# Optimization experiments

Measured on AMD Instinct MI355X. Metric: run time of the kernel, lower is better.

The kernel has to match this reference:

```python
import jax, jax.numpy as jnp
import numpy as np

N, DIM, HID, NCLS, E = 100000, 256, 16, 64, 3200000
NEG_SLOPE = 0.2


def setup_inputs() -> dict:
    key = jax.random.key(0)
    ks = jax.random.split(key, 10)
    x = jax.random.normal(ks[0], (N, DIM), dtype=jnp.float32)
    edge_index = jax.random.randint(ks[1], (2, E), 0, N, dtype=jnp.int64)
    # GATConv params (heads=1): glorot-ish scaled normals
    W1 = jax.random.normal(ks[2], (DIM, HID), dtype=jnp.float32) / np.sqrt(DIM)
    a_src1 = jax.random.normal(ks[3], (HID,), dtype=jnp.float32) / np.sqrt(HID)
    a_dst1 = jax.random.normal(ks[4], (HID,), dtype=jnp.float32) / np.sqrt(HID)
    b1 = jnp.zeros((HID,), dtype=jnp.float32)
    W2 = jax.random.normal(ks[5], (HID, NCLS), dtype=jnp.float32) / np.sqrt(HID)
    a_src2 = jax.random.normal(ks[6], (NCLS,), dtype=jnp.float32) / np.sqrt(NCLS)
    a_dst2 = jax.random.normal(ks[7], (NCLS,), dtype=jnp.float32) / np.sqrt(NCLS)
    b2 = jnp.zeros((NCLS,), dtype=jnp.float32)
    return {"x": x, "edge_index": edge_index, "W1": W1, "a_src1": a_src1,
            "a_dst1": a_dst1, "b1": b1, "W2": W2, "a_src2": a_src2,
            "a_dst2": a_dst2, "b2": b2}


def gat_conv(x, src, dst, W, a_s, a_d, b, n):
    # PyG GATConv, heads=1: h = x W; e_ij = LeakyReLU(a_s.h_j + a_d.h_i)
    h = x @ W                                   # [N, out]
    alpha_s = h @ a_s                           # [N]
    alpha_d = h @ a_d                           # [N]
    e = jax.nn.leaky_relu(alpha_s[src] + alpha_d[dst], NEG_SLOPE)  # [E]
    # softmax over edges grouped by destination node
    m = jax.ops.segment_max(e, dst, num_segments=n)
    m = jnp.where(jnp.isfinite(m), m, 0.0)
    ee = jnp.exp(e - m[dst])
    denom = jax.ops.segment_sum(ee, dst, num_segments=n)
    alpha = ee / denom[dst]                     # self-loops guarantee denom > 0
    out = jax.ops.segment_sum(h[src] * alpha[:, None], dst, num_segments=n)
    return out + b


def reference(x, edge_index, W1, a_src1, a_dst1, b1, W2, a_src2, a_dst2, b2):
    n = x.shape[0]
    loop = jnp.arange(n, dtype=edge_index.dtype)
    src = jnp.concatenate([edge_index[0], loop])  # add self-loops (PyG default)
    dst = jnp.concatenate([edge_index[1], loop])
    h = jax.nn.relu(gat_conv(x, src, dst, W1, a_src1, a_dst1, b1, n))
    # F.dropout treated as identity (inference / deterministic reference)
    out = gat_conv(h, src, dst, W2, a_src2, a_dst2, b2, n)
    return jax.nn.log_softmax(out, axis=1)
```

## Files before the change

### kernel.cpp

```cpp
#include <hip/hip_runtime.h>
#include <hip/hip_fp16.h>


#define DIM 256
#define HID 16
#define NCLS 64
#define NEG 0.2f
#define P1_CHUNK 4096
#define KITER 16
#define CAP 8704

typedef _Float16 f16x8 __attribute__((ext_vector_type(8)));
typedef float f32x4 __attribute__((ext_vector_type(4)));

#define PIN4(v) asm volatile("" : "+v"(v.x), "+v"(v.y), "+v"(v.z), "+v"(v.w))

__device__ __forceinline__ float lrelu(float v) { return v >= 0.f ? v : NEG * v; }

__device__ __forceinline__ uint4 pack_half8(const float* v) {
    __half2 p0 = __floats2half2_rn(v[0], v[1]);
    __half2 p1 = __floats2half2_rn(v[2], v[3]);
    __half2 p2 = __floats2half2_rn(v[4], v[5]);
    __half2 p3 = __floats2half2_rn(v[6], v[7]);
    return make_uint4(*(unsigned*)&p0, *(unsigned*)&p1, *(unsigned*)&p2, *(unsigned*)&p3);
}

__device__ __forceinline__ void unpack_half8(uint4 u, float* f) {
    float2 f0 = __half22float2(*(__half2*)&u.x);
    float2 f1 = __half22float2(*(__half2*)&u.y);
    float2 f2 = __half22float2(*(__half2*)&u.z);
    float2 f3 = __half22float2(*(__half2*)&u.w);
    f[0] = f0.x; f[1] = f0.y; f[2] = f1.x; f[3] = f1.y;
    f[4] = f2.x; f[5] = f2.y; f[6] = f3.x; f[7] = f3.y;
}

__global__ void vsd_kernel(const float* __restrict__ W2, const float* __restrict__ as2,
                           const float* __restrict__ ad2, float* __restrict__ vsd,
                           int* __restrict__ bkt_cnt, int* __restrict__ bkt_cur, int capb) {
    int t = threadIdx.x;
    bkt_cnt[t] = 0;
    bkt_cur[t] = capb ? t * capb : 0;
    if (t < 32) {
        int j = t & 15;
        const float* a = (t < 16) ? as2 : ad2;
        float s = 0.f;
        for (int c = 0; c < NCLS; ++c) s += W2[j * NCLS + c] * a[c];
        vsd[t] = s;
    }
}


__global__ __launch_bounds__(256) void p0_hist(const int* __restrict__ dst, int E,
                                               int* __restrict__ bkt_cnt) {
    __shared__ int hist[512];
    int t = threadIdx.x;
    for (int i = t; i < 512; i += 256) hist[i] = 0;
    __syncthreads();
    int base = blockIdx.x * P1_CHUNK;
#pragma unroll
    for (int k = 0; k < KITER; ++k) {
        int idx = base + k * 256 + t;
        if (idx < E) atomicAdd(&hist[dst[idx] >> 8], 1);
    }
    __syncthreads();
    for (int i = t; i < 512; i += 256)
        if (hist[i]) atomicAdd(&bkt_cnt[i], hist[i]);
}

__global__ void scanb(int* __restrict__ bkt_cnt, int* __restrict__ bkt_cur,
                      int* __restrict__ bkt_base, int nb) {
    __shared__ int lds[512];
    int t = threadIdx.x;
    int v = (t < nb) ? bkt_cnt[t] : 0;
    lds[t] = v;
    __syncthreads();
    for (int o = 1; o < 512; o <<= 1) {
        int x = (t >= o) ? lds[t - o] : 0;
        __syncthreads();
        lds[t] += x;
        __syncthreads();
    }
    if (t < nb) {
        int e = lds[t] - v;
        bkt_base[t] = e;
        bkt_cur[t] = e;
    }
}

struct H1S {
    _Float16 w1t[16][264];
    _Float16 hst[4][16][16];
};

__global__ __launch_bounds__(256) void p1h1_kernel(
    const int* __restrict__ ei, int E, int* __restrict__ bkt_cur,
    int* __restrict__ coarse, int nS, int h1blk, int capb,
    const float* __restrict__ x, const float* __restrict__ W1,
    const float* __restrict__ asw, const float* __restrict__ adw,
    uint4* __restrict__ h1h, float* __restrict__ as1, float* __restrict__ ad1, int n) {
    __shared__ union __align__(16) { int hist[512]; H1S h1; } sm;
    int t = threadIdx.x;
    int bid = blockIdx.x;
    int total = nS + h1blk;
    int f0 = (int)(((long long)bid * h1blk) / total);
    int f1 = (int)(((long long)(bid + 1) * h1blk) / total);
    if (f1 == f0) {
        int sb = bid - f0;
        int base = sb * P1_CHUNK;
        int sarr[KITER], darr[KITER];
        for (int i = t; i < 512; i += 256) sm.hist[i] = 0;
        bool e4 = ((E & 3) == 0);
#pragma unroll
        for (int k = 0; k < KITER / 4; ++k) {
            int idx = base + (k * 256 + t) * 4;
            if (e4 && idx + 3 < E) {
                int4 s4 = *(const int4*)&ei[idx];
                int4 d4 = *(const int4*)&ei[E + idx];
                sarr[4 * k] = s4.x; sarr[4 * k + 1] = s4.y;
                sarr[4 * k + 2] = s4.z; sarr[4 * k + 3] = s4.w;
                darr[4 * k] = d4.x; darr[4 * k + 1] = d4.y;
                darr[4 * k + 2] = d4.z; darr[4 * k + 3] = d4.w;
            } else {
#pragma unroll
                for (int j = 0; j < 4; ++j) {
                    int id2 = idx + j;
                    if (id2 < E) { sarr[4 * k + j] = ei[id2]; darr[4 * k + j] = ei[E + id2]; }
                    else darr[4 * k + j] = -1;
                }
            }
        }
        __syncthreads();
#pragma unroll
        for (int k = 0; k < KITER; ++k)
            if (darr[k] >= 0) atomicAdd(&sm.hist[darr[k] >> 8], 1);
        __syncthreads();
        for (int b = t; b < 512; b += 256) {
            int c = sm.hist[b];
            sm.hist[b] = c ? atomicAdd(&bkt_cur[b], c) : 0;
        }
        __syncthreads();
#pragma unroll
        for (int k = 0; k < KITER; ++k) {
            int d = darr[k];
            if (d >= 0) {
                int bk = d >> 8;
                int pos = atomicAdd(&sm.hist[bk], 1);
                if (capb) pos = min(pos, (bk + 1) * capb - 1);
                coarse[pos] = (sarr[k] << 8) | (d & 255);
            }
        }
    } else {
        int hb = f0;
        {
            const float* row = W1 + t * HID;
#pragma unroll
            for (int nn2 = 0; nn2 < 16; ++nn2)
                sm.h1.w1t[nn2][t] = (_Float16)row[nn2];
        }
        __syncthreads();
        int lane = t & 63, wave = t >> 6;
        int q = lane >> 4, nn = lane & 15;
        float asv = asw[nn], adv = adw[nn];
#pragma unroll 1
        for (int it = 0; it < 4; ++it) {
            int nb = hb * 256 + wave * 64 + it * 16;
            int node = nb + nn;
            const float* xr = x + (size_t)min(node, n - 1) * DIM;
            float4 st[16];
#pragma unroll
            for (int s = 0; s < 8; ++s) {
                int kb = s * 32 + q * 8;
                st[2 * s]     = *(const float4*)(xr + kb);
                st[2 * s + 1] = *(const float4*)(xr + kb + 4);
            }
#pragma unroll
            for (int i = 0; i < 16; ++i) PIN4(st[i]);
            f32x4 acc = {0.f, 0.f, 0.f, 0.f};
#pragma unroll
            for (int s = 0; s < 8; ++s) {
                int kb = s * 32 + q * 8;
                f16x8 bf = *(const f16x8*)&sm.h1.w1t[nn][kb];
                float4 a0 = st[2 * s], a1 = st[2 * s + 1];
                f16x8 af;
                af[0] = (_Float16)a0.x; af[1] = (_Float16)a0.y;
                af[2] = (_Float16)a0.z; af[3] = (_Float16)a0.w;
                af[4] = (_Float16)a1.x; af[5] = (_Float16)a1.y;
                af[6] = (_Float16)a1.z; af[7] = (_Float16)a1.w;
                acc = __builtin_amdgcn_mfma_f32_16x16x32_f16(af, bf, acc, 0, 0, 0);
            }
            if (nb < n) {
#pragma unroll
                for (int r = 0; r < 4; ++r) {
                    float v = acc[r];
                    sm.h1.hst[wave][q * 4 + r][nn] = (_Float16)v;
                    float t1 = v * asv, t2 = v * adv;
#pragma unroll
                    for (int mm = 1; mm < 16; mm <<= 1) {
                        t1 += __shfl_xor(t1, mm, 64);
                        t2 += __shfl_xor(t2, mm, 64);
                    }
                    if (nn == 0) {
                        int nd = nb + q * 4 + r;
                        if (nd < n) { as1[nd] = t1; ad1[nd] = t2; }
                    }
                }
                __builtin_amdgcn_s_waitcnt(0);
                if (lane < 32) {
                    int nl = lane >> 1, jq = lane & 1;
                    int nd = nb + nl;
                    if (nd < n)
                        h1h[(size_t)nd * 2 + jq] = *(const uint4*)&sm.h1.hst[wave][nl][jq * 8];
                }
            }
        }
    }
}

__global__ __launch_bounds__(512) void p2_fine(const int* __restrict__ coarse,
                                               const int* __restrict__ bkt_base,
                                               const int* __restrict__ bkt_cnt,
                                               const int* __restrict__ bkt_cur,
                                               int* __restrict__ csr, int* __restrict__ row_ptr,
                                               int* __restrict__ deg, int n, int capb) {
    __shared__ int cnt[256];
    __shared__ int off[256];
    __shared__ int csr_loc[CAP];
    int b = blockIdx.x;
    int t = threadIdx.x;
    int m, wbase;
    if (capb) {
        int* sc = csr_loc;
        int cv = bkt_cur[t] - t * capb;
        sc[t] = cv;
        __syncthreads();
        for (int o = 1; o < 512; o <<= 1) {
            int xg = (t >= o) ? sc[t - o] : 0;
            __syncthreads();
            sc[t] += xg;
            __syncthreads();
        }
        m = bkt_cur[b] - b * capb;
        wbase = sc[b] - m;
        __syncthreads();
    } else {
        m = bkt_cnt[b];
        wbase = bkt_base[b];
    }
    int rbase = capb ? b * capb : wbase;
    if (t < 256) cnt[t] = 0;
    __syncthreads();
    for (int i = t; i < m; i += 512) atomicAdd(&cnt[coarse[rbase + i] & 255], 1);
    __syncthreads();
    int v = 0;
    if (t < 256) { v = cnt[t]; off[t] = v; }
    __syncthreads();
    for (int o = 1; o < 256; o <<= 1) {
        int xg = (t >= o && t < 256) ? off[t - o] : 0;
        __syncthreads();
        if (t < 256) off[t] += xg;
        __syncthreads();
    }
    if (t < 256) {
        int excl = off[t] - v;
        int node = b * 256 + t;
        if (node < n) {
            row_ptr[node] = wbase + excl;
            deg[node] = v;
        }
        cnt[t] = excl;
    }
    __syncthreads();
    if (m <= CAP) {
        for (int i = t; i < m; i += 512) {
            int rec = coarse[rbase + i];
            int pos = atomicAdd(&cnt[rec & 255], 1);
            csr_loc[pos] = rec >> 8;
        }
        __syncthreads();
        for (int i = t; i < m; i += 512) csr[wbase + i] = csr_loc[i];
    } else {
        for (int i = t; i < m; i += 512) {
            int rec = coarse[rbase + i];
            int pos = atomicAdd(&cnt[rec & 255], 1);
            csr[wbase + pos] = rec >> 8;
        }
    }
}


__device__ __forceinline__ void agg_core(
    const uint4* __restrict__ hh, const float* __restrict__ as, float adi,
    int node, int start, int cnt, const int* __restrict__ csr,
    int lg, int eq, int jq, int gbase, float* acc, float& denomv) {
    float w0 = __expf(lrelu(as[node] + adi));
    float w0s = (eq == 0) ? w0 : 0.f;
    float hs[8];
    unpack_half8(hh[(size_t)node * 2 + jq], hs);
#pragma unroll
    for (int i = 0; i < 8; ++i) acc[i] = w0s * hs[i];
    float denom = w0s;
    int sv = (lg < cnt) ? csr[start + lg] : 0;
    float av = as[sv];
    for (int q0 = 0; q0 < cnt; q0 += 16) {
        int nq = q0 + 16 + lg;
        int nsv = (nq < cnt) ? csr[start + nq] : 0;
        float nav = as[nsv];
        float wv = (q0 + lg < cnt) ? __expf(lrelu(av + adi)) : 0.f;
        int s0 = __shfl(sv, gbase + eq, 64);
        int s1 = __shfl(sv, gbase + 8 + eq, 64);
        float wA = __shfl(wv, gbase + eq, 64);
        float wB = __shfl(wv, gbase + 8 + eq, 64);
        uint4 u0 = hh[(size_t)s0 * 2 + jq];
        uint4 u1 = hh[(size_t)s1 * 2 + jq];
        denom += wA + wB;
        float h0[8], h1v[8];
        unpack_half8(u0, h0);
        unpack_half8(u1, h1v);
#pragma unroll
        for (int i = 0; i < 8; ++i) acc[i] += wA * h0[i] + wB * h1v[i];
        sv = nsv;
        av = nav;
    }
#pragma unroll
    for (int m = 2; m <= 8; m <<= 1) {
#pragma unroll
        for (int i = 0; i < 8; ++i) acc[i] += __shfl_xor(acc[i], m, 64);
        denom += __shfl_xor(denom, m, 64);
    }
    denomv = denom;
}

__global__ __launch_bounds__(256) void agg1_kernel(
    const uint4* __restrict__ hh, const float* __restrict__ as, const float* __restrict__ ad,
    const int* __restrict__ row_ptr, const int* __restrict__ deg, const int* __restrict__ csr,
    const float* __restrict__ bias, const float* __restrict__ vsd,
    uint4* __restrict__ outh, float* __restrict__ as_out, float* __restrict__ ad_out,
    int n) {
    int t = threadIdx.x;
    int node = blockIdx.x * 16 + (t >> 4);
    if (node >= n) return;
    int lg = t & 15, jq = lg & 1, eq = lg >> 1, gbase = t & 48;
    float adi = ad[node];
    float acc[8];
    float denom;
    agg_core(hh, as, adi, node, row_ptr[node], deg[node], csr, lg, eq, jq, gbase, acc, denom);
    float inv = 1.f / denom;
    const float* bj = bias + jq * 8;
    float val[8];
#pragma unroll
    for (int i = 0; i < 8; ++i) val[i] = fmaxf(acc[i] * inv + bj[i], 0.f);
    if (eq == 0) outh[(size_t)node * 2 + jq] = pack_half8(val);
    const float* vs = vsd + jq * 8;
    const float* vd = vsd + 16 + jq * 8;
    float t1 = 0.f, t2 = 0.f;
#pragma unroll
    for (int i = 0; i < 8; ++i) { t1 += val[i] * vs[i]; t2 += val[i] * vd[i]; }
    t1 += __shfl_xor(t1, 1, 64);
    t2 += __shfl_xor(t2, 1, 64);
    if (lg == 0) { as_out[node] = t1; ad_out[node] = t2; }
}

__global__ __launch_bounds__(256) void agg2_final_kernel(
    const uint4* __restrict__ hh, const float* __restrict__ as, const float* __restrict__ ad,
    const int* __restrict__ row_ptr, const int* __restrict__ deg, const int* __restrict__ csr,
    const float* __restrict__ W2, const float* __restrict__ b2,
    float* __restrict__ out, int n) {
    __shared__ float a2s[16 * HID];
    __shared__ float w2s[HID * NCLS];
    __shared__ float b2s[NCLS];
    int t = threadIdx.x;
    for (int i = t; i < HID * NCLS; i += 256) w2s[i] = W2[i];
    if (t < NCLS) b2s[t] = b2[t];
    int g = t >> 4;
    int node = blockIdx.x * 16 + g;
    int lg = t & 15, jq = lg & 1, eq = lg >> 1, gbase = t & 48;
    if (node < n) {
        float adi = ad[node];
        float acc[8];
        float denom;
        agg_core(hh, as, adi, node, row_ptr[node], deg[node], csr, lg, eq, jq, gbase, acc, denom);
        float inv = 1.f / denom;
        if (eq == 0) {
            float* dst = &a2s[g * HID + jq * 8];
            *(float4*)dst = make_float4(acc[0] * inv, acc[1] * inv, acc[2] * inv, acc[3] * inv);
            *(float4*)(dst + 4) = make_float4(acc[4] * inv, acc[5] * inv, acc[6] * inv, acc[7] * inv);
        }
    }
    __syncthreads();
    int wv = t >> 6;
    int c = t & 63;
#pragma unroll
    for (int i = 0; i < 4; ++i) {
        int nl = i * 4 + wv;
        int gn = blockIdx.x * 16 + nl;
        if (gn >= n) continue;
        const float* ar = &a2s[nl * HID];
        float v = b2s[c];
#pragma unroll
        for (int j = 0; j < HID; ++j) v += ar[j] * w2s[j * NCLS + c];
        float mx = v;
#pragma unroll
        for (int off = 1; off < 64; off <<= 1) mx = fmaxf(mx, __shfl_xor(mx, off, 64));
        float ex = __expf(v - mx);
        float s = ex;
#pragma unroll
        for (int off = 1; off < 64; off <<= 1) s += __shfl_xor(s, off, 64);
        out[(size_t)gn * NCLS + c] = (v - mx) - __logf(s);
    }
}

extern "C" void kernel_launch(void* const* d_in, const int* in_sizes, int n_in,
                              void* d_out, int out_size, void* d_ws, size_t ws_size,
                              hipStream_t stream) {
    const float* x    = (const float*)d_in[0];
    const int*   ei   = (const int*)d_in[1];
    const float* W1   = (const float*)d_in[2];
    const float* a_s1 = (const float*)d_in[3];
    const float* a_d1 = (const float*)d_in[4];
    const float* b1   = (const float*)d_in[5];
    const float* W2   = (const float*)d_in[6];
    const float* a_s2 = (const float*)d_in[7];
    const float* a_d2 = (const float*)d_in[8];
    const float* b2   = (const float*)d_in[9];
    float* out = (float*)d_out;

    const int N = in_sizes[0] / DIM;
    const int E = in_sizes[1] / 2;
    const int NB = (N + 255) >> 8;
    const int nS = (E + P1_CHUNK - 1) / P1_CHUNK;
    const int h1blk = (N + 255) / 256;

    char* p = (char*)d_ws;
    auto alloc = [&](size_t bytes) {
        char* r = p;
        p += (bytes + 255) & ~(size_t)255;
        return r;
    };
    int*   bkt_cnt  = (int*)alloc(512 * 4);
    int*   bkt_base = (int*)alloc(512 * 4);
    int*   bkt_cur  = (int*)alloc(512 * 4);
    int*   csr      = (int*)alloc((size_t)E * 4);
    int*   row_ptr  = (int*)alloc((size_t)N * 4);
    int*   deg      = (int*)alloc((size_t)N * 4);
    float* as1      = (float*)alloc((size_t)N * 4);
    float* ad1      = (float*)alloc((size_t)N * 4);
    float* as2      = (float*)alloc((size_t)N * 4);
    float* ad2      = (float*)alloc((size_t)N * 4);
    float* vsd      = (float*)alloc(32 * 4);
    uint4* h1h      = (uint4*)alloc((size_t)N * 32);
    uint4* hreluh   = (uint4*)alloc((size_t)N * 32);

    int capb = 10240;
    size_t used = (size_t)(p - (char*)d_ws);
    size_t pad_bytes = (size_t)512 * capb * 4;
    int* coarse;
    if (ws_size - used >= pad_bytes) {
        coarse = (int*)alloc(pad_bytes);
    } else {
        capb = 0;
        coarse = (int*)alloc((size_t)E * 4);
    }

    vsd_kernel<<<1, 512, 0, stream>>>(W2, a_s2, a_d2, vsd, bkt_cnt, bkt_cur, capb);
    if (!capb) {
        p0_hist<<<nS, 256, 0, stream>>>(ei + E, E, bkt_cnt);
        scanb<<<1, 512, 0, stream>>>(bkt_cnt, bkt_cur, bkt_base, NB);
    }
    p1h1_kernel<<<nS + h1blk, 256, 0, stream>>>(ei, E, bkt_cur, coarse, nS, h1blk, capb,
                                                x, W1, a_s1, a_d1, h1h, as1, ad1, N);
    p2_fine<<<NB, 512, 0, stream>>>(coarse, bkt_base, bkt_cnt, bkt_cur,
                                    csr, row_ptr, deg, N, capb);
    agg1_kernel<<<(N + 15) / 16, 256, 0, stream>>>(h1h, as1, ad1, row_ptr, deg, csr,
                                                   b1, vsd, hreluh, as2, ad2, N);
    agg2_final_kernel<<<(N + 15) / 16, 256, 0, stream>>>(hreluh, as2, ad2, row_ptr, deg, csr,
                                                         W2, b2, out, N);
}
```

Baseline: 304.9 us.

## Fuse CSR fine bucketing with layer-1 aggregation reading neighbors from LDS

Merges the fine bucket-sort kernel and the first-layer aggregation into one kernel. Each block builds the CSR for its 256 destination nodes and then aggregates them directly from the shared-memory CSR copy, avoiding a kernel launch and a global re-read of csr/row_ptr/deg. The aggregation loop now processes 32 edges per iteration without software prefetch, and the x loads in the h1 GEMM are replaced by inline-asm global loads with an explicit waitcnt. The risk is that only 512 blocks of 512 threads handle all layer-1 aggregation, which reduces parallelism and latency hiding compared with the previous separate grid of about 6250 blocks.

```diff
diff --git a/kernel.cpp b/kernel.cpp
--- a/kernel.cpp
+++ b/kernel.cpp
@@ -12,8 +12,6 @@
 
 typedef _Float16 f16x8 __attribute__((ext_vector_type(8)));
 typedef float f32x4 __attribute__((ext_vector_type(4)));
-
-#define PIN4(v) asm volatile("" : "+v"(v.x), "+v"(v.y), "+v"(v.z), "+v"(v.w))
 
 __device__ __forceinline__ float lrelu(float v) { return v >= 0.f ? v : NEG * v; }
 
@@ -166,26 +164,28 @@
             int nb = hb * 256 + wave * 64 + it * 16;
             int node = nb + nn;
             const float* xr = x + (size_t)min(node, n - 1) * DIM;
-            float4 st[16];
+            f32x4 st[16];
 #pragma unroll
             for (int s = 0; s < 8; ++s) {
                 int kb = s * 32 + q * 8;
-                st[2 * s]     = *(const float4*)(xr + kb);
-                st[2 * s + 1] = *(const float4*)(xr + kb + 4);
+                asm volatile("global_load_dwordx4 %0, %1, off"
+                             : "=v"(st[2 * s]) : "v"(xr + kb) : "memory");
+                asm volatile("global_load_dwordx4 %0, %1, off"
+                             : "=v"(st[2 * s + 1]) : "v"(xr + kb + 4) : "memory");
             }
-#pragma unroll
-            for (int i = 0; i < 16; ++i) PIN4(st[i]);
+            asm volatile("s_waitcnt vmcnt(0)" ::: "memory");
+            __builtin_amdgcn_sched_barrier(0);
             f32x4 acc = {0.f, 0.f, 0.f, 0.f};
 #pragma unroll
             for (int s = 0; s < 8; ++s) {
                 int kb = s * 32 + q * 8;
                 f16x8 bf = *(const f16x8*)&sm.h1.w1t[nn][kb];
-                float4 a0 = st[2 * s], a1 = st[2 * s + 1];
+                f32x4 a0 = st[2 * s], a1 = st[2 * s + 1];
                 f16x8 af;
-                af[0] = (_Float16)a0.x; af[1] = (_Float16)a0.y;
-                af[2] = (_Float16)a0.z; af[3] = (_Float16)a0.w;
-                af[4] = (_Float16)a1.x; af[5] = (_Float16)a1.y;
-                af[6] = (_Float16)a1.z; af[7] = (_Float16)a1.w;
+                af[0] = (_Float16)a0[0]; af[1] = (_Float16)a0[1];
+                af[2] = (_Float16)a0[2]; af[3] = (_Float16)a0[3];
+                af[4] = (_Float16)a1[0]; af[5] = (_Float16)a1[1];
+                af[6] = (_Float16)a1[2]; af[7] = (_Float16)a1[3];
                 acc = __builtin_amdgcn_mfma_f32_16x16x32_f16(af, bf, acc, 0, 0, 0);
             }
             if (nb < n) {
@@ -216,14 +216,72 @@
     }
 }
 
-__global__ __launch_bounds__(512) void p2_fine(const int* __restrict__ coarse,
-                                               const int* __restrict__ bkt_base,
-                                               const int* __restrict__ bkt_cnt,
-                                               const int* __restrict__ bkt_cur,
-                                               int* __restrict__ csr, int* __restrict__ row_ptr,
-                                               int* __restrict__ deg, int n, int capb) {
+
+__device__ __forceinline__ void agg_core(
+    const uint4* __restrict__ hh, const float* __restrict__ as, float adi,
+    int node, int start, int cnt, const int* csr,
+    int lg, int eq, int jq, int gbase, float* acc, float& denomv) {
+    float w0 = __expf(lrelu(as[node] + adi));
+    float w0s = (eq == 0) ? w0 : 0.f;
+    float hs[8];
+    unpack_half8(hh[(size_t)node * 2 + jq], hs);
+#pragma unroll
+    for (int i = 0; i < 8; ++i) acc[i] = w0s * hs[i];
+    float denom = w0s;
+#pragma unroll 1
+    for (int q0 = 0; q0 < cnt; q0 += 32) {
+        int i0 = q0 + lg, i1 = q0 + 16 + lg;
+        int svA = (i0 < cnt) ? csr[start + i0] : 0;
+        int svB = (i1 < cnt) ? csr[start + i1] : 0;
+        float avA = as[svA];
+        float avB = as[svB];
+        float wvA = (i0 < cnt) ? __expf(lrelu(avA + adi)) : 0.f;
+        float wvB = (i1 < cnt) ? __expf(lrelu(avB + adi)) : 0.f;
+        int sl0 = gbase + eq, sl1 = gbase + 8 + eq;
+        int s0 = __shfl(svA, sl0, 64);
+        int s1 = __shfl(svA, sl1, 64);
+        int s2 = __shfl(svB, sl0, 64);
+        int s3 = __shfl(svB, sl1, 64);
+        float wA = __shfl(wvA, sl0, 64);
+        float wB = __shfl(wvA, sl1, 64);
+        float wC = __shfl(wvB, sl0, 64);
+        float wD = __shfl(wvB, sl1, 64);
+        uint4 u0 = hh[(size_t)s0 * 2 + jq];
+        uint4 u1 = hh[(size_t)s1 * 2 + jq];
+        uint4 u2 = hh[(size_t)s2 * 2 + jq];
+        uint4 u3 = hh[(size_t)s3 * 2 + jq];
+        denom += wA + wB + wC + wD;
+        float h0[8], h1v[8], h2[8], h3[8];
+        unpack_half8(u0, h0);
+        unpack_half8(u1, h1v);
+        unpack_half8(u2, h2);
+        unpack_half8(u3, h3);
+#pragma unroll
+        for (int i = 0; i < 8; ++i)
+            acc[i] += wA * h0[i] + wB * h1v[i] + wC * h2[i] + wD * h3[i];
+    }
+#pragma unroll
+    for (int m = 2; m <= 8; m <<= 1) {
+#pragma unroll
+        for (int i = 0; i < 8; ++i) acc[i] += __shfl_xor(acc[i], m, 64);
+        denom += __shfl_xor(denom, m, 64);
+    }
+    denomv = denom;
+}
+
+__global__ __launch_bounds__(512) void p2agg1_kernel(
+    const int* __restrict__ coarse, const int* __restrict__ bkt_base,
+    const int* __restrict__ bkt_cnt, const int* __restrict__ bkt_cur,
+    int* __restrict__ csr, int* __restrict__ row_ptr, int* __restrict__ deg,
+    int n, int capb,
+    const uint4* __restrict__ hh, const float* __restrict__ as,
+    const float* __restrict__ ad, const float* __restrict__ bias,
+    const float* __restrict__ vsd, uint4* __restrict__ outh,
+    float* __restrict__ as_out, float* __restrict__ ad_out) {
     __shared__ int cnt[256];
     __shared__ int off[256];
+    __shared__ int lstart[256];
+    __shared__ int ldeg[256];
     __shared__ int csr_loc[CAP];
     int b = blockIdx.x;
     int t = threadIdx.x;
@@ -260,6 +318,7 @@
         if (t < 256) off[t] += xg;
         __syncthreads();
     }
+    bool inlds = (m <= CAP);
     if (t < 256) {
         int excl = off[t] - v;
         int node = b * 256 + t;
@@ -267,10 +326,12 @@
             row_ptr[node] = wbase + excl;
             deg[node] = v;
         }
+        lstart[t] = excl;
+        ldeg[t] = v;
         cnt[t] = excl;
     }
     __syncthreads();
-    if (m <= CAP) {
+    if (inlds) {
         for (int i = t; i < m; i += 512) {
             int rec = coarse[rbase + i];
             int pos = atomicAdd(&cnt[rec & 255], 1);
@@ -284,80 +345,34 @@
             int pos = atomicAdd(&cnt[rec & 255], 1);
             csr[wbase + pos] = rec >> 8;
         }
-    }
-}
-
-
-__device__ __forceinline__ void agg_core(
-    const uint4* __restrict__ hh, const float* __restrict__ as, float adi,
-    int node, int start, int cnt, const int* __restrict__ csr,
-    int lg, int eq, int jq, int gbase, float* acc, float& denomv) {
-    float w0 = __expf(lrelu(as[node] + adi));
-    float w0s = (eq == 0) ? w0 : 0.f;
-    float hs[8];
-    unpack_half8(hh[(size_t)node * 2 + jq], hs);
-#pragma unroll
-    for (int i = 0; i < 8; ++i) acc[i] = w0s * hs[i];
-    float denom = w0s;
-    int sv = (lg < cnt) ? csr[start + lg] : 0;
-    float av = as[sv];
-    for (int q0 = 0; q0 < cnt; q0 += 16) {
-        int nq = q0 + 16 + lg;
-        int nsv = (nq < cnt) ? csr[start + nq] : 0;
-        float nav = as[nsv];
-        float wv = (q0 + lg < cnt) ? __expf(lrelu(av + adi)) : 0.f;
-        int s0 = __shfl(sv, gbase + eq, 64);
-        int s1 = __shfl(sv, gbase + 8 + eq, 64);
-        float wA = __shfl(wv, gbase + eq, 64);
-        float wB = __shfl(wv, gbase + 8 + eq, 64);
-        uint4 u0 = hh[(size_t)s0 * 2 + jq];
-        uint4 u1 = hh[(size_t)s1 * 2 + jq];
-        denom += wA + wB;
-        float h0[8], h1v[8];
-        unpack_half8(u0, h0);
-        unpack_half8(u1, h1v);
-#pragma unroll
-        for (int i = 0; i < 8; ++i) acc[i] += wA * h0[i] + wB * h1v[i];
-        sv = nsv;
-        av = nav;
-    }
-#pragma unroll
-    for (int m = 2; m <= 8; m <<= 1) {
-#pragma unroll
-        for (int i = 0; i < 8; ++i) acc[i] += __shfl_xor(acc[i], m, 64);
-        denom += __shfl_xor(denom, m, 64);
-    }
-    denomv = denom;
-}
-
-__global__ __launch_bounds__(256) void agg1_kernel(
-    const uint4* __restrict__ hh, const float* __restrict__ as, const float* __restrict__ ad,
-    const int* __restrict__ row_ptr, const int* __restrict__ deg, const int* __restrict__ csr,
-    const float* __restrict__ bias, const float* __restrict__ vsd,
-    uint4* __restrict__ outh, float* __restrict__ as_out, float* __restrict__ ad_out,
-    int n) {
-    int t = threadIdx.x;
-    int node = blockIdx.x * 16 + (t >> 4);
-    if (node >= n) return;
+        __syncthreads();
+    }
     int lg = t & 15, jq = lg & 1, eq = lg >> 1, gbase = t & 48;
-    float adi = ad[node];
-    float acc[8];
-    float denom;
-    agg_core(hh, as, adi, node, row_ptr[node], deg[node], csr, lg, eq, jq, gbase, acc, denom);
-    float inv = 1.f / denom;
-    const float* bj = bias + jq * 8;
-    float val[8];
-#pragma unroll
-    for (int i = 0; i < 8; ++i) val[i] = fmaxf(acc[i] * inv + bj[i], 0.f);
-    if (eq == 0) outh[(size_t)node * 2 + jq] = pack_half8(val);
-    const float* vs = vsd + jq * 8;
-    const float* vd = vsd + 16 + jq * 8;
-    float t1 = 0.f, t2 = 0.f;
-#pragma unroll
-    for (int i = 0; i < 8; ++i) { t1 += val[i] * vs[i]; t2 += val[i] * vd[i]; }
-    t1 += __shfl_xor(t1, 1, 64);
-    t2 += __shfl_xor(t2, 1, 64);
-    if (lg == 0) { as_out[node] = t1; ad_out[node] = t2; }
+    const int* csrp = inlds ? (const int*)csr_loc : (const int*)(csr + wbase);
+#pragma unroll 1
+    for (int pass = 0; pass < 8; ++pass) {
+        int nl = pass * 32 + (t >> 4);
+        int node = b * 256 + nl;
+        if (node >= n) continue;
+        float adi = ad[node];
+        float acc[8];
+        float denom;
+        agg_core(hh, as, adi, node, lstart[nl], ldeg[nl], csrp, lg, eq, jq, gbase, acc, denom);
+        float inv = 1.f / denom;
+        const float* bj = bias + jq * 8;
+        float val[8];
+#pragma unroll
+        for (int i = 0; i < 8; ++i) val[i] = fmaxf(acc[i] * inv + bj[i], 0.f);
+        if (eq == 0) outh[(size_t)node * 2 + jq] = pack_half8(val);
+        const float* vs = vsd + jq * 8;
+        const float* vd = vsd + 16 + jq * 8;
+        float t1 = 0.f, t2 = 0.f;
+#pragma unroll
+        for (int i = 0; i < 8; ++i) { t1 += val[i] * vs[i]; t2 += val[i] * vd[i]; }
+        t1 += __shfl_xor(t1, 1, 64);
+        t2 += __shfl_xor(t2, 1, 64);
+        if (lg == 0) { as_out[node] = t1; ad_out[node] = t2; }
+    }
 }
 
 __global__ __launch_bounds__(256) void agg2_final_kernel(
@@ -468,10 +483,9 @@
     }
     p1h1_kernel<<<nS + h1blk, 256, 0, stream>>>(ei, E, bkt_cur, coarse, nS, h1blk, capb,
                                                 x, W1, a_s1, a_d1, h1h, as1, ad1, N);
-    p2_fine<<<NB, 512, 0, stream>>>(coarse, bkt_base, bkt_cnt, bkt_cur,
-                                    csr, row_ptr, deg, N, capb);
-    agg1_kernel<<<(N + 15) / 16, 256, 0, stream>>>(h1h, as1, ad1, row_ptr, deg, csr,
-                                                   b1, vsd, hreluh, as2, ad2, N);
+    p2agg1_kernel<<<NB, 512, 0, stream>>>(coarse, bkt_base, bkt_cnt, bkt_cur,
+                                          csr, row_ptr, deg, N, capb,
+                                          h1h, as1, ad1, b1, vsd, hreluh, as2, ad2);
     agg2_final_kernel<<<(N + 15) / 16, 256, 0, stream>>>(hreluh, as2, ad2, row_ptr, deg, csr,
                                                          W2, b2, out, N);
 }
```

New measurement: 313.0 us. +2.7%, slower.

## Co-locate alpha_src with node features and software-pipeline H1 loads and gathers

Applied to the files above, without the earlier changes.

Widens each node's half-precision feature record from 32 to 64 bytes and stores the per-node source attention score inside it. The aggregation gather then fetches the score and the features from the same cache line instead of doing a separate random access into an as array. The aggregation loop now handles 32 neighbors per iteration without cross-iteration prefetch. The H1 projection loop is double-buffered with sched barriers so x loads for the next tile overlap the MFMA work on the current one. The cost is doubled feature storage and more bytes per random gather line, plus higher register pressure from the two load buffers.

```diff
diff --git a/kernel.cpp b/kernel.cpp
--- a/kernel.cpp
+++ b/kernel.cpp
@@ -12,8 +12,6 @@
 
 typedef _Float16 f16x8 __attribute__((ext_vector_type(8)));
 typedef float f32x4 __attribute__((ext_vector_type(4)));
-
-#define PIN4(v) asm volatile("" : "+v"(v.x), "+v"(v.y), "+v"(v.z), "+v"(v.w))
 
 __device__ __forceinline__ float lrelu(float v) { return v >= 0.f ? v : NEG * v; }
 
@@ -97,7 +95,7 @@
     int* __restrict__ coarse, int nS, int h1blk, int capb,
     const float* __restrict__ x, const float* __restrict__ W1,
     const float* __restrict__ asw, const float* __restrict__ adw,
-    uint4* __restrict__ h1h, float* __restrict__ as1, float* __restrict__ ad1, int n) {
+    uint4* __restrict__ h1h, float* __restrict__ ad1, int n) {
     __shared__ union __align__(16) { int hist[512]; H1S h1; } sm;
     int t = threadIdx.x;
     int bid = blockIdx.x;
@@ -161,20 +159,21 @@
         int lane = t & 63, wave = t >> 6;
         int q = lane >> 4, nn = lane & 15;
         float asv = asw[nn], adv = adw[nn];
-#pragma unroll 1
-        for (int it = 0; it < 4; ++it) {
+
+        float4 st0[16], st1[16];
+        auto ISSUE = [&](float4 (&st)[16], int it) {
             int nb = hb * 256 + wave * 64 + it * 16;
             int node = nb + nn;
             const float* xr = x + (size_t)min(node, n - 1) * DIM;
-            float4 st[16];
 #pragma unroll
             for (int s = 0; s < 8; ++s) {
                 int kb = s * 32 + q * 8;
                 st[2 * s]     = *(const float4*)(xr + kb);
                 st[2 * s + 1] = *(const float4*)(xr + kb + 4);
             }
-#pragma unroll
-            for (int i = 0; i < 16; ++i) PIN4(st[i]);
+        };
+        auto COMPUTE = [&](const float4 (&st)[16], int it) {
+            int nb = hb * 256 + wave * 64 + it * 16;
             f32x4 acc = {0.f, 0.f, 0.f, 0.f};
 #pragma unroll
             for (int s = 0; s < 8; ++s) {
@@ -201,18 +200,36 @@
                     }
                     if (nn == 0) {
                         int nd = nb + q * 4 + r;
-                        if (nd < n) { as1[nd] = t1; ad1[nd] = t2; }
+                        if (nd < n) {
+                            ((float*)(h1h + (size_t)nd * 4))[8] = t1;
+                            ad1[nd] = t2;
+                        }
                     }
                 }
-                __builtin_amdgcn_s_waitcnt(0);
+                asm volatile("s_waitcnt lgkmcnt(0)" ::: "memory");
                 if (lane < 32) {
                     int nl = lane >> 1, jq = lane & 1;
                     int nd = nb + nl;
                     if (nd < n)
-                        h1h[(size_t)nd * 2 + jq] = *(const uint4*)&sm.h1.hst[wave][nl][jq * 8];
+                        h1h[(size_t)nd * 4 + jq] = *(const uint4*)&sm.h1.hst[wave][nl][jq * 8];
                 }
             }
-        }
+        };
+        ISSUE(st0, 0);
+        __builtin_amdgcn_sched_barrier(0);
+        ISSUE(st1, 1);
+        __builtin_amdgcn_sched_barrier(0);
+        COMPUTE(st0, 0);
+        __builtin_amdgcn_sched_barrier(0);
+        ISSUE(st0, 2);
+        __builtin_amdgcn_sched_barrier(0);
+        COMPUTE(st1, 1);
+        __builtin_amdgcn_sched_barrier(0);
+        ISSUE(st1, 3);
+        __builtin_amdgcn_sched_barrier(0);
+        COMPUTE(st0, 2);
+        __builtin_amdgcn_sched_barrier(0);
+        COMPUTE(st1, 3);
     }
 }
 
@@ -289,37 +306,49 @@
 
 
 __device__ __forceinline__ void agg_core(
-    const uint4* __restrict__ hh, const float* __restrict__ as, float adi,
+    const uint4* __restrict__ hh, float adi,
     int node, int start, int cnt, const int* __restrict__ csr,
     int lg, int eq, int jq, int gbase, float* acc, float& denomv) {
-    float w0 = __expf(lrelu(as[node] + adi));
+    const float* hhf = (const float*)hh;
+    float asn = hhf[(size_t)node * 16 + 8];
+    float w0 = __expf(lrelu(asn + adi));
     float w0s = (eq == 0) ? w0 : 0.f;
     float hs[8];
-    unpack_half8(hh[(size_t)node * 2 + jq], hs);
+    unpack_half8(hh[(size_t)node * 4 + jq], hs);
 #pragma unroll
     for (int i = 0; i < 8; ++i) acc[i] = w0s * hs[i];
     float denom = w0s;
-    int sv = (lg < cnt) ? csr[start + lg] : 0;
-    float av = as[sv];
-    for (int q0 = 0; q0 < cnt; q0 += 16) {
-        int nq = q0 + 16 + lg;
-        int nsv = (nq < cnt) ? csr[start + nq] : 0;
-        float nav = as[nsv];
-        float wv = (q0 + lg < cnt) ? __expf(lrelu(av + adi)) : 0.f;
-        int s0 = __shfl(sv, gbase + eq, 64);
-        int s1 = __shfl(sv, gbase + 8 + eq, 64);
-        float wA = __shfl(wv, gbase + eq, 64);
-        float wB = __shfl(wv, gbase + 8 + eq, 64);
-        uint4 u0 = hh[(size_t)s0 * 2 + jq];
-        uint4 u1 = hh[(size_t)s1 * 2 + jq];
-        denom += wA + wB;
-        float h0[8], h1v[8];
+#pragma unroll 1
+    for (int q0 = 0; q0 < cnt; q0 += 32) {
+        int i0 = q0 + lg, i1 = q0 + 16 + lg;
+        int svA = (i0 < cnt) ? csr[start + i0] : 0;
+        int svB = (i1 < cnt) ? csr[start + i1] : 0;
+        float avA = hhf[(size_t)svA * 16 + 8];
+        float avB = hhf[(size_t)svB * 16 + 8];
+        float wvA = (i0 < cnt) ? __expf(lrelu(avA + adi)) : 0.f;
+        float wvB = (i1 < cnt) ? __expf(lrelu(avB + adi)) : 0.f;
+        int sl0 = gbase + eq, sl1 = gbase + 8 + eq;
+        int s0 = __shfl(svA, sl0, 64);
+        int s1 = __shfl(svA, sl1, 64);
+        int s2 = __shfl(svB, sl0, 64);
+        int s3 = __shfl(svB, sl1, 64);
+        float wA = __shfl(wvA, sl0, 64);
+        float wB = __shfl(wvA, sl1, 64);
+        float wC = __shfl(wvB, sl0, 64);
+        float wD = __shfl(wvB, sl1, 64);
+        uint4 u0 = hh[(size_t)s0 * 4 + jq];
+        uint4 u1 = hh[(size_t)s1 * 4 + jq];
+        uint4 u2 = hh[(size_t)s2 * 4 + jq];
+        uint4 u3 = hh[(size_t)s3 * 4 + jq];
+        denom += wA + wB + wC + wD;
+        float h0[8], h1v[8], h2[8], h3[8];
         unpack_half8(u0, h0);
         unpack_half8(u1, h1v);
-#pragma unroll
-        for (int i = 0; i < 8; ++i) acc[i] += wA * h0[i] + wB * h1v[i];
-        sv = nsv;
-        av = nav;
+        unpack_half8(u2, h2);
+        unpack_half8(u3, h3);
+#pragma unroll
+        for (int i = 0; i < 8; ++i)
+            acc[i] += wA * h0[i] + wB * h1v[i] + wC * h2[i] + wD * h3[i];
     }
 #pragma unroll
     for (int m = 2; m <= 8; m <<= 1) {
@@ -331,11 +360,10 @@
 }
 
 __global__ __launch_bounds__(256) void agg1_kernel(
-    const uint4* __restrict__ hh, const float* __restrict__ as, const float* __restrict__ ad,
+    const uint4* __restrict__ hh, const float* __restrict__ ad,
     const int* __restrict__ row_ptr, const int* __restrict__ deg, const int* __restrict__ csr,
     const float* __restrict__ bias, const float* __restrict__ vsd,
-    uint4* __restrict__ outh, float* __restrict__ as_out, float* __restrict__ ad_out,
-    int n) {
+    uint4* __restrict__ outh, float* __restrict__ ad_out, int n) {
     int t = threadIdx.x;
     int node = blockIdx.x * 16 + (t >> 4);
     if (node >= n) return;
@@ -343,13 +371,13 @@
     float adi = ad[node];
     float acc[8];
     float denom;
-    agg_core(hh, as, adi, node, row_ptr[node], deg[node], csr, lg, eq, jq, gbase, acc, denom);
+    agg_core(hh, adi, node, row_ptr[node], deg[node], csr, lg, eq, jq, gbase, acc, denom);
     float inv = 1.f / denom;
     const float* bj = bias + jq * 8;
     float val[8];
 #pragma unroll
     for (int i = 0; i < 8; ++i) val[i] = fmaxf(acc[i] * inv + bj[i], 0.f);
-    if (eq == 0) outh[(size_t)node * 2 + jq] = pack_half8(val);
+    if (eq == 0) outh[(size_t)node * 4 + jq] = pack_half8(val);
     const float* vs = vsd + jq * 8;
     const float* vd = vsd + 16 + jq * 8;
     float t1 = 0.f, t2 = 0.f;
@@ -357,11 +385,14 @@
     for (int i = 0; i < 8; ++i) { t1 += val[i] * vs[i]; t2 += val[i] * vd[i]; }
     t1 += __shfl_xor(t1, 1, 64);
     t2 += __shfl_xor(t2, 1, 64);
-    if (lg == 0) { as_out[node] = t1; ad_out[node] = t2; }
+    if (lg == 0) {
+        ((float*)(outh + (size_t)node * 4))[8] = t1;
+        ad_out[node] = t2;
+    }
 }
 
 __global__ __launch_bounds__(256) void agg2_final_kernel(
-    const uint4* __restrict__ hh, const float* __restrict__ as, const float* __restrict__ ad,
+    const uint4* __restrict__ hh, const float* __restrict__ ad,
     const int* __restrict__ row_ptr, const int* __restrict__ deg, const int* __restrict__ csr,
     const float* __restrict__ W2, const float* __restrict__ b2,
     float* __restrict__ out, int n) {
@@ -378,7 +409,7 @@
         float adi = ad[node];
         float acc[8];
         float denom;
-        agg_core(hh, as, adi, node, row_ptr[node], deg[node], csr, lg, eq, jq, gbase, acc, denom);
+        agg_core(hh, adi, node, row_ptr[node], deg[node], csr, lg, eq, jq, gbase, acc, denom);
         float inv = 1.f / denom;
         if (eq == 0) {
             float* dst = &a2s[g * HID + jq * 8];
@@ -442,13 +473,11 @@
     int*   csr      = (int*)alloc((size_t)E * 4);
     int*   row_ptr  = (int*)alloc((size_t)N * 4);
     int*   deg      = (int*)alloc((size_t)N * 4);
-    float* as1      = (float*)alloc((size_t)N * 4);
     float* ad1      = (float*)alloc((size_t)N * 4);
-    float* as2      = (float*)alloc((size_t)N * 4);
     float* ad2      = (float*)alloc((size_t)N * 4);
     float* vsd      = (float*)alloc(32 * 4);
-    uint4* h1h      = (uint4*)alloc((size_t)N * 32);
-    uint4* hreluh   = (uint4*)alloc((size_t)N * 32);
+    uint4* h1h      = (uint4*)alloc((size_t)N * 64);
+    uint4* hreluh   = (uint4*)alloc((size_t)N * 64);
 
     int capb = 10240;
     size_t used = (size_t)(p - (char*)d_ws);
@@ -467,11 +496,11 @@
         scanb<<<1, 512, 0, stream>>>(bkt_cnt, bkt_cur, bkt_base, NB);
     }
     p1h1_kernel<<<nS + h1blk, 256, 0, stream>>>(ei, E, bkt_cur, coarse, nS, h1blk, capb,
-                                                x, W1, a_s1, a_d1, h1h, as1, ad1, N);
+                                                x, W1, a_s1, a_d1, h1h, ad1, N);
     p2_fine<<<NB, 512, 0, stream>>>(coarse, bkt_base, bkt_cnt, bkt_cur,
                                     csr, row_ptr, deg, N, capb);
-    agg1_kernel<<<(N + 15) / 16, 256, 0, stream>>>(h1h, as1, ad1, row_ptr, deg, csr,
-                                                   b1, vsd, hreluh, as2, ad2, N);
-    agg2_final_kernel<<<(N + 15) / 16, 256, 0, stream>>>(hreluh, as2, ad2, row_ptr, deg, csr,
+    agg1_kernel<<<(N + 15) / 16, 256, 0, stream>>>(h1h, ad1, row_ptr, deg, csr,
+                                                   b1, vsd, hreluh, ad2, N);
+    agg2_final_kernel<<<(N + 15) / 16, 256, 0, stream>>>(hreluh, ad2, row_ptr, deg, csr,
                                                          W2, b2, out, N);
 }
```

Result: slower. 321.4 us (+5.4%).

## Recompute attention scores from gathered features instead of separate score arrays

Applied to the files above, without the earlier changes.

Drops the precomputed per-node alpha_src/alpha_dst arrays. Each aggregation kernel now recomputes the source score as a dot product of the fp16 neighbor features it already gathers, and the destination score from the node's own features. This removes the dependent gather of the score array per edge, the score writes in the h1 and agg1 kernels, and four N-sized buffers. The edge loop now processes 32 edges per iteration instead of 16, and the register-pinning asm is removed. In exchange it adds per-edge dot-product math and shuffles, and source scores come from fp16-rounded features, which may change numerics slightly.

```diff
diff --git a/kernel.cpp b/kernel.cpp
--- a/kernel.cpp
+++ b/kernel.cpp
@@ -12,8 +12,6 @@
 
 typedef _Float16 f16x8 __attribute__((ext_vector_type(8)));
 typedef float f32x4 __attribute__((ext_vector_type(4)));
-
-#define PIN4(v) asm volatile("" : "+v"(v.x), "+v"(v.y), "+v"(v.z), "+v"(v.w))
 
 __device__ __forceinline__ float lrelu(float v) { return v >= 0.f ? v : NEG * v; }
 
@@ -96,8 +94,7 @@
     const int* __restrict__ ei, int E, int* __restrict__ bkt_cur,
     int* __restrict__ coarse, int nS, int h1blk, int capb,
     const float* __restrict__ x, const float* __restrict__ W1,
-    const float* __restrict__ asw, const float* __restrict__ adw,
-    uint4* __restrict__ h1h, float* __restrict__ as1, float* __restrict__ ad1, int n) {
+    uint4* __restrict__ h1h, int n) {
     __shared__ union __align__(16) { int hist[512]; H1S h1; } sm;
     int t = threadIdx.x;
     int bid = blockIdx.x;
@@ -160,7 +157,6 @@
         __syncthreads();
         int lane = t & 63, wave = t >> 6;
         int q = lane >> 4, nn = lane & 15;
-        float asv = asw[nn], adv = adw[nn];
 #pragma unroll 1
         for (int it = 0; it < 4; ++it) {
             int nb = hb * 256 + wave * 64 + it * 16;
@@ -173,8 +169,6 @@
                 st[2 * s]     = *(const float4*)(xr + kb);
                 st[2 * s + 1] = *(const float4*)(xr + kb + 4);
             }
-#pragma unroll
-            for (int i = 0; i < 16; ++i) PIN4(st[i]);
             f32x4 acc = {0.f, 0.f, 0.f, 0.f};
 #pragma unroll
             for (int s = 0; s < 8; ++s) {
@@ -190,20 +184,8 @@
             }
             if (nb < n) {
 #pragma unroll
-                for (int r = 0; r < 4; ++r) {
-                    float v = acc[r];
-                    sm.h1.hst[wave][q * 4 + r][nn] = (_Float16)v;
-                    float t1 = v * asv, t2 = v * adv;
-#pragma unroll
-                    for (int mm = 1; mm < 16; mm <<= 1) {
-                        t1 += __shfl_xor(t1, mm, 64);
-                        t2 += __shfl_xor(t2, mm, 64);
-                    }
-                    if (nn == 0) {
-                        int nd = nb + q * 4 + r;
-                        if (nd < n) { as1[nd] = t1; ad1[nd] = t2; }
-                    }
-                }
+                for (int r = 0; r < 4; ++r)
+                    sm.h1.hst[wave][q * 4 + r][nn] = (_Float16)acc[r];
                 __builtin_amdgcn_s_waitcnt(0);
                 if (lane < 32) {
                     int nl = lane >> 1, jq = lane & 1;
@@ -289,37 +271,64 @@
 
 
 __device__ __forceinline__ void agg_core(
-    const uint4* __restrict__ hh, const float* __restrict__ as, float adi,
+    const uint4* __restrict__ hh, const float* aw, const float* dw,
     int node, int start, int cnt, const int* __restrict__ csr,
-    int lg, int eq, int jq, int gbase, float* acc, float& denomv) {
-    float w0 = __expf(lrelu(as[node] + adi));
+    int lg, int eq, int jq, int gbase, float* acc, float* hs, float& denomv) {
+    unpack_half8(hh[(size_t)node * 2 + jq], hs);
+    float asn = 0.f, adn = 0.f;
+#pragma unroll
+    for (int i = 0; i < 8; ++i) { asn += hs[i] * aw[i]; adn += hs[i] * dw[i]; }
+    asn += __shfl_xor(asn, 1, 64);
+    adn += __shfl_xor(adn, 1, 64);
+    float adi = adn;
+    float w0 = __expf(lrelu(asn + adi));
     float w0s = (eq == 0) ? w0 : 0.f;
-    float hs[8];
-    unpack_half8(hh[(size_t)node * 2 + jq], hs);
 #pragma unroll
     for (int i = 0; i < 8; ++i) acc[i] = w0s * hs[i];
     float denom = w0s;
-    int sv = (lg < cnt) ? csr[start + lg] : 0;
-    float av = as[sv];
-    for (int q0 = 0; q0 < cnt; q0 += 16) {
-        int nq = q0 + 16 + lg;
-        int nsv = (nq < cnt) ? csr[start + nq] : 0;
-        float nav = as[nsv];
-        float wv = (q0 + lg < cnt) ? __expf(lrelu(av + adi)) : 0.f;
-        int s0 = __shfl(sv, gbase + eq, 64);
-        int s1 = __shfl(sv, gbase + 8 + eq, 64);
-        float wA = __shfl(wv, gbase + eq, 64);
-        float wB = __shfl(wv, gbase + 8 + eq, 64);
+    int svA = (lg < cnt) ? csr[start + lg] : 0;
+    int svB = (16 + lg < cnt) ? csr[start + 16 + lg] : 0;
+#pragma unroll 1
+    for (int q0 = 0; q0 < cnt; q0 += 32) {
+        int nA = q0 + 32 + lg, nB = q0 + 48 + lg;
+        int nsvA = (nA < cnt) ? csr[start + nA] : 0;
+        int nsvB = (nB < cnt) ? csr[start + nB] : 0;
+        int sl0 = gbase + eq, sl1 = gbase + 8 + eq;
+        int s0 = __shfl(svA, sl0, 64);
+        int s1 = __shfl(svA, sl1, 64);
+        int s2 = __shfl(svB, sl0, 64);
+        int s3 = __shfl(svB, sl1, 64);
         uint4 u0 = hh[(size_t)s0 * 2 + jq];
         uint4 u1 = hh[(size_t)s1 * 2 + jq];
-        denom += wA + wB;
-        float h0[8], h1v[8];
+        uint4 u2 = hh[(size_t)s2 * 2 + jq];
+        uint4 u3 = hh[(size_t)s3 * 2 + jq];
+        float h0[8], h1v[8], h2[8], h3[8];
         unpack_half8(u0, h0);
         unpack_half8(u1, h1v);
-#pragma unroll
-        for (int i = 0; i < 8; ++i) acc[i] += wA * h0[i] + wB * h1v[i];
-        sv = nsv;
-        av = nav;
+        unpack_half8(u2, h2);
+        unpack_half8(u3, h3);
+        float p0 = 0.f, p1 = 0.f, p2 = 0.f, p3 = 0.f;
+#pragma unroll
+        for (int i = 0; i < 8; ++i) {
+            p0 += h0[i] * aw[i];
+            p1 += h1v[i] * aw[i];
+            p2 += h2[i] * aw[i];
+            p3 += h3[i] * aw[i];
+        }
+        p0 += __shfl_xor(p0, 1, 64);
+        p1 += __shfl_xor(p1, 1, 64);
+        p2 += __shfl_xor(p2, 1, 64);
+        p3 += __shfl_xor(p3, 1, 64);
+        float wA = (q0 + eq < cnt)      ? __expf(lrelu(p0 + adi)) : 0.f;
+        float wB = (q0 + 8 + eq < cnt)  ? __expf(lrelu(p1 + adi)) : 0.f;
+        float wC = (q0 + 16 + eq < cnt) ? __expf(lrelu(p2 + adi)) : 0.f;
+        float wD = (q0 + 24 + eq < cnt) ? __expf(lrelu(p3 + adi)) : 0.f;
+        denom += wA + wB + wC + wD;
+#pragma unroll
+        for (int i = 0; i < 8; ++i)
+            acc[i] += wA * h0[i] + wB * h1v[i] + wC * h2[i] + wD * h3[i];
+        svA = nsvA;
+        svB = nsvB;
     }
 #pragma unroll
     for (int m = 2; m <= 8; m <<= 1) {
@@ -331,38 +340,31 @@
 }
 
 __global__ __launch_bounds__(256) void agg1_kernel(
-    const uint4* __restrict__ hh, const float* __restrict__ as, const float* __restrict__ ad,
+    const uint4* __restrict__ hh,
     const int* __restrict__ row_ptr, const int* __restrict__ deg, const int* __restrict__ csr,
-    const float* __restrict__ bias, const float* __restrict__ vsd,
-    uint4* __restrict__ outh, float* __restrict__ as_out, float* __restrict__ ad_out,
-    int n) {
+    const float* __restrict__ as1, const float* __restrict__ ad1,
+    const float* __restrict__ bias, uint4* __restrict__ outh, int n) {
     int t = threadIdx.x;
     int node = blockIdx.x * 16 + (t >> 4);
     if (node >= n) return;
     int lg = t & 15, jq = lg & 1, eq = lg >> 1, gbase = t & 48;
-    float adi = ad[node];
-    float acc[8];
+    float aw[8], dw[8];
+#pragma unroll
+    for (int i = 0; i < 8; ++i) { aw[i] = as1[jq * 8 + i]; dw[i] = ad1[jq * 8 + i]; }
+    float acc[8], hs[8];
     float denom;
-    agg_core(hh, as, adi, node, row_ptr[node], deg[node], csr, lg, eq, jq, gbase, acc, denom);
+    agg_core(hh, aw, dw, node, row_ptr[node], deg[node], csr, lg, eq, jq, gbase, acc, hs, denom);
     float inv = 1.f / denom;
-    const float* bj = bias + jq * 8;
     float val[8];
 #pragma unroll
-    for (int i = 0; i < 8; ++i) val[i] = fmaxf(acc[i] * inv + bj[i], 0.f);
+    for (int i = 0; i < 8; ++i) val[i] = fmaxf(acc[i] * inv + bias[jq * 8 + i], 0.f);
     if (eq == 0) outh[(size_t)node * 2 + jq] = pack_half8(val);
-    const float* vs = vsd + jq * 8;
-    const float* vd = vsd + 16 + jq * 8;
-    float t1 = 0.f, t2 = 0.f;
-#pragma unroll
-    for (int i = 0; i < 8; ++i) { t1 += val[i] * vs[i]; t2 += val[i] * vd[i]; }
-    t1 += __shfl_xor(t1, 1, 64);
-    t2 += __shfl_xor(t2, 1, 64);
-    if (lg == 0) { as_out[node] = t1; ad_out[node] = t2; }
 }
 
 __global__ __launch_bounds__(256) void agg2_final_kernel(
-    const uint4* __restrict__ hh, const float* __restrict__ as, const float* __restrict__ ad,
+    const uint4* __restrict__ hh,
     const int* __restrict__ row_ptr, const int* __restrict__ deg, const int* __restrict__ csr,
+    const float* __restrict__ vsd,
     const float* __restrict__ W2, const float* __restrict__ b2,
     float* __restrict__ out, int n) {
     __shared__ float a2s[16 * HID];
@@ -375,10 +377,12 @@
     int node = blockIdx.x * 16 + g;
     int lg = t & 15, jq = lg & 1, eq = lg >> 1, gbase = t & 48;
     if (node < n) {
-        float adi = ad[node];
-        float acc[8];
+        float aw[8], dw[8];
+#pragma unroll
+        for (int i = 0; i < 8; ++i) { aw[i] = vsd[jq * 8 + i]; dw[i] = vsd[16 + jq * 8 + i]; }
+        float acc[8], hs[8];
         float denom;
-        agg_core(hh, as, adi, node, row_ptr[node], deg[node], csr, lg, eq, jq, gbase, acc, denom);
+        agg_core(hh, aw, dw, node, row_ptr[node], deg[node], csr, lg, eq, jq, gbase, acc, hs, denom);
         float inv = 1.f / denom;
         if (eq == 0) {
             float* dst = &a2s[g * HID + jq * 8];
@@ -442,10 +446,6 @@
     int*   csr      = (int*)alloc((size_t)E * 4);
     int*   row_ptr  = (int*)alloc((size_t)N * 4);
     int*   deg      = (int*)alloc((size_t)N * 4);
-    float* as1      = (float*)alloc((size_t)N * 4);
-    float* ad1      = (float*)alloc((size_t)N * 4);
-    float* as2      = (float*)alloc((size_t)N * 4);
-    float* ad2      = (float*)alloc((size_t)N * 4);
     float* vsd      = (float*)alloc(32 * 4);
     uint4* h1h      = (uint4*)alloc((size_t)N * 32);
     uint4* hreluh   = (uint4*)alloc((size_t)N * 32);
@@ -467,11 +467,11 @@
         scanb<<<1, 512, 0, stream>>>(bkt_cnt, bkt_cur, bkt_base, NB);
     }
     p1h1_kernel<<<nS + h1blk, 256, 0, stream>>>(ei, E, bkt_cur, coarse, nS, h1blk, capb,
-                                                x, W1, a_s1, a_d1, h1h, as1, ad1, N);
+                                                x, W1, h1h, N);
     p2_fine<<<NB, 512, 0, stream>>>(coarse, bkt_base, bkt_cnt, bkt_cur,
                                     csr, row_ptr, deg, N, capb);
-    agg1_kernel<<<(N + 15) / 16, 256, 0, stream>>>(h1h, as1, ad1, row_ptr, deg, csr,
-                                                   b1, vsd, hreluh, as2, ad2, N);
-    agg2_final_kernel<<<(N + 15) / 16, 256, 0, stream>>>(hreluh, as2, ad2, row_ptr, deg, csr,
-                                                         W2, b2, out, N);
-}
+    agg1_kernel<<<(N + 15) / 16, 256, 0, stream>>>(h1h, row_ptr, deg, csr,
+                                                   a_s1, a_d1, b1, hreluh, N);
+    agg2_final_kernel<<<(N + 15) / 16, 256, 0, stream>>>(hreluh, row_ptr, deg, csr,
+                                                         vsd, W2, b2, out, N);
+}
```

Result: no change. 299.8 us (-1.7%).
